# Performance work log

Measured on AMD Instinct MI355X. Metric: run time of the kernel, lower is better.

Reference implementation:

```python
import jax, jax.numpy as jnp
import numpy as np

N_NODES = 100000


def setup_inputs() -> dict:
    key = jax.random.key(0)
    k1, k2, k3, k4, k5 = jax.random.split(key, 5)
    n_edges = 1600000
    d_in, d_out = 128, 128
    input_features = jax.random.normal(k1, (N_NODES, d_in), dtype=jnp.float32)
    weight = jax.random.normal(k2, (d_in, d_out), dtype=jnp.float32) * (1.0 / np.sqrt(d_out))
    edge_vals = jax.random.uniform(k3, (n_edges,), dtype=jnp.float32)
    edge_src = jax.random.randint(k4, (n_edges,), 0, N_NODES, dtype=jnp.int32)
    edge_dst = jax.random.randint(k5, (n_edges,), 0, N_NODES, dtype=jnp.int32)
    return {
        "input_features": input_features,
        "weight": weight,
        "edge_vals": edge_vals,
        "edge_src": edge_src,
        "edge_dst": edge_dst,
    }


def reference(input_features, weight, edge_vals, edge_src, edge_dst):
    neg_slope = 0.0
    # dense transform: support = X @ W  -> [N, d_out]
    support = input_features @ weight
    # sparse SpMM: out[dst] += val * support[src]  (COO adjacency)
    msgs = edge_vals[:, None] * support[edge_src]  # [E, d_out]
    output = jax.ops.segment_sum(msgs, edge_dst, num_segments=N_NODES)
    # leaky_relu with negative_slope = neg_slope (0 -> relu)
    return jnp.where(output >= 0, output, neg_slope * output)
```

## Files before the change

### kernel.cpp

```cpp
#include <hip/hip_runtime.h>
#include <hip/hip_bf16.h>


#define D 128
#define NB_SHIFT 6
#define BNODES 64
#define MAXB 2048
#define CAPB 1408
#define RPT 6
#define XSTR 136
#define NFILL 256
#define GROWS 128

using bf16x8 = __attribute__((ext_vector_type(8))) short;
using f32x4  = __attribute__((ext_vector_type(4))) float;

__device__ inline unsigned short f2bf(float f) {
    unsigned u = __float_as_uint(f);
    u += 0x7fffu + ((u >> 16) & 1u);
    return (unsigned short)(u >> 16);
}

__global__ __launch_bounds__(256) void wtrans(const float* __restrict__ W,
                                              unsigned short* __restrict__ WT,
                                              int* cursor, int nb) {
    const int t = threadIdx.x, b = blockIdx.x;
    const int n  = (b << 4) | (t & 15);
    const int k0 = (t >> 4) << 3;
#pragma unroll
    for (int k = k0; k < k0 + 8; ++k)
        WT[n * D + k] = f2bf(W[k * D + n]);
    if (b == 0)
        for (int i = t; i < nb; i += 256) cursor[i] = 0;
}

#define SMEM_BYTES (GROWS * XSTR * 2 + 128 * XSTR * 2 + GROWS * 4)

__device__ void gemm_path(const float* __restrict__ X,
                          const unsigned short* __restrict__ WT,
                          unsigned char* __restrict__ S8,
                          float* __restrict__ scaleArr,
                          int nRows, int blk, char* smem) {
    unsigned short* Xl = (unsigned short*)smem;
    unsigned short* Wl = (unsigned short*)(smem + GROWS * XSTR * 2);
    int* rowAmaxI = (int*)(smem + GROWS * XSTR * 2 + 128 * XSTR * 2);

    const int t = threadIdx.x;
    const int row0 = blk * GROWS;

    if (t < GROWS) rowAmaxI[t] = 0;

    const uint4* WT4 = (const uint4*)WT;
    uint4* Wl4 = (uint4*)Wl;
#pragma unroll
    for (int i = t; i < 2048; i += 1024) {
        int n = i >> 4, kc8 = i & 15;
        Wl4[n * (XSTR / 8) + kc8] = WT4[i];
    }

    const float4* X4 = (const float4*)X;
    ushort4* Xl4 = (ushort4*)Xl;
#pragma unroll
    for (int i = t; i < 4096; i += 1024) {
        int r = i >> 5, c = i & 31;
        int gr = row0 + r;
        float4 v = make_float4(0.f, 0.f, 0.f, 0.f);
        if (gr < nRows) v = X4[(size_t)gr * 32 + c];
        ushort4 p;
        p.x = f2bf(v.x); p.y = f2bf(v.y); p.z = f2bf(v.z); p.w = f2bf(v.w);
        Xl4[r * (XSTR / 4) + c] = p;
    }
    __syncthreads();

    const int wv = t >> 6, lane = t & 63;
    const int m = lane & 15, quad = lane >> 4;
    const int m0  = (wv & 7) << 4;
    const int nt0 = (wv >> 3) << 2;

    f32x4 acc[4];
    f32x4 z = {0.f, 0.f, 0.f, 0.f};
#pragma unroll
    for (int nt = 0; nt < 4; ++nt) acc[nt] = z;

#pragma unroll
    for (int kc = 0; kc < 4; ++kc) {
        bf16x8 a = *(const bf16x8*)(Xl + (m0 + m) * XSTR + kc * 32 + quad * 8);
#pragma unroll
        for (int nt = 0; nt < 4; ++nt) {
            bf16x8 b = *(const bf16x8*)(Wl + ((nt0 + nt) * 16 + m) * XSTR + kc * 32 + quad * 8);
            acc[nt] = __builtin_amdgcn_mfma_f32_16x16x32_bf16(a, b, acc[nt], 0, 0, 0);
        }
    }

#pragma unroll
    for (int r = 0; r < 4; ++r) {
        float lm = fabsf(acc[0][r]);
        lm = fmaxf(lm, fabsf(acc[1][r]));
        lm = fmaxf(lm, fabsf(acc[2][r]));
        lm = fmaxf(lm, fabsf(acc[3][r]));
        atomicMax(&rowAmaxI[m0 + quad * 4 + r], __float_as_int(lm));
    }
    __syncthreads();

#pragma unroll
    for (int r = 0; r < 4; ++r) {
        const int row = m0 + quad * 4 + r;
        const int gr = row0 + row;
        const float rm = __int_as_float(rowAmaxI[row]);
        const float inv = rm > 0.f ? 127.f / rm : 0.f;
        if (gr < nRows) {
#pragma unroll
            for (int nt = 0; nt < 4; ++nt) {
                int q = __float2int_rn(acc[nt][r] * inv) + 128;
                S8[(size_t)gr * D + (nt0 + nt) * 16 + m] = (unsigned char)q;
            }
            if (m == 0 && nt0 == 0)
                scaleArr[gr] = rm * (1.f / 127.f);
        }
    }
}

__device__ void fill2_path(const int* __restrict__ src,
                           const int* __restrict__ dst,
                           const float* __restrict__ vals,
                           int* gcursor, int2* __restrict__ epk,
                           int E, int nb, int blk, char* smem) {
    int* h   = (int*)smem;
    int* cur = (int*)(smem + MAXB * 4);
    const int t = threadIdx.x;
    for (int i = t; i < nb; i += 1024) h[i] = 0;
    __syncthreads();

    int chunk = (E + NFILL - 1) / NFILL;
    chunk = (chunk + 3) & ~3;
    const int s0 = min(E, blk * chunk);
    const int s1 = min(E, s0 + chunk);
    const int vend = s0 + ((s1 - s0) & ~3);

    const int e0 = s0 + (t << 2);
    const int e1 = e0 + 4096;
    int4 rs0, rd0, rs1, rd1;
    float4 rv0, rv1;
    const bool has0 = (e0 + 4 <= vend);
    const bool has1 = (e1 + 4 <= vend);
    if (has0) {
        rd0 = *(const int4*)(dst + e0);
        rs0 = *(const int4*)(src + e0);
        rv0 = *(const float4*)(vals + e0);
        atomicAdd(&h[rd0.x >> NB_SHIFT], 1);
        atomicAdd(&h[rd0.y >> NB_SHIFT], 1);
        atomicAdd(&h[rd0.z >> NB_SHIFT], 1);
        atomicAdd(&h[rd0.w >> NB_SHIFT], 1);
    }
    if (has1) {
        rd1 = *(const int4*)(dst + e1);
        rs1 = *(const int4*)(src + e1);
        rv1 = *(const float4*)(vals + e1);
        atomicAdd(&h[rd1.x >> NB_SHIFT], 1);
        atomicAdd(&h[rd1.y >> NB_SHIFT], 1);
        atomicAdd(&h[rd1.z >> NB_SHIFT], 1);
        atomicAdd(&h[rd1.w >> NB_SHIFT], 1);
    }
    for (int e = vend + t; e < s1; e += 1024)
        atomicAdd(&h[dst[e] >> NB_SHIFT], 1);
    __syncthreads();

    for (int i = t; i < nb; i += 1024) {
        int c = h[i];
        cur[i] = c ? (i * CAPB + atomicAdd(&gcursor[i], c)) : 0;
    }
    __syncthreads();

    if (has0) {
        int p0 = atomicAdd(&cur[rd0.x >> NB_SHIFT], 1);
        int p1 = atomicAdd(&cur[rd0.y >> NB_SHIFT], 1);
        int p2 = atomicAdd(&cur[rd0.z >> NB_SHIFT], 1);
        int p3 = atomicAdd(&cur[rd0.w >> NB_SHIFT], 1);
        epk[p0] = make_int2(rs0.x | ((rd0.x & (BNODES - 1)) << 20), __float_as_int(rv0.x));
        epk[p1] = make_int2(rs0.y | ((rd0.y & (BNODES - 1)) << 20), __float_as_int(rv0.y));
        epk[p2] = make_int2(rs0.z | ((rd0.z & (BNODES - 1)) << 20), __float_as_int(rv0.z));
        epk[p3] = make_int2(rs0.w | ((rd0.w & (BNODES - 1)) << 20), __float_as_int(rv0.w));
    }
    if (has1) {
        int p0 = atomicAdd(&cur[rd1.x >> NB_SHIFT], 1);
        int p1 = atomicAdd(&cur[rd1.y >> NB_SHIFT], 1);
        int p2 = atomicAdd(&cur[rd1.z >> NB_SHIFT], 1);
        int p3 = atomicAdd(&cur[rd1.w >> NB_SHIFT], 1);
        epk[p0] = make_int2(rs1.x | ((rd1.x & (BNODES - 1)) << 20), __float_as_int(rv1.x));
        epk[p1] = make_int2(rs1.y | ((rd1.y & (BNODES - 1)) << 20), __float_as_int(rv1.y));
        epk[p2] = make_int2(rs1.z | ((rd1.z & (BNODES - 1)) << 20), __float_as_int(rv1.z));
        epk[p3] = make_int2(rs1.w | ((rd1.w & (BNODES - 1)) << 20), __float_as_int(rv1.w));
    }
    for (int e = vend + t; e < s1; e += 1024) {
        int d = dst[e];
        int pos = atomicAdd(&cur[d >> NB_SHIFT], 1);
        epk[pos] = make_int2(src[e] | ((d & (BNODES - 1)) << 20), __float_as_int(vals[e]));
    }
}

__global__ __launch_bounds__(1024, 8) void fused_pre(const float* __restrict__ X,
                                                     const unsigned short* __restrict__ WT,
                                                     unsigned char* __restrict__ S8,
                                                     float* __restrict__ scaleArr,
                                                     int nRows,
                                                     const int* __restrict__ src,
                                                     const int* __restrict__ dst,
                                                     const float* __restrict__ vals,
                                                     int* gcursor, int2* __restrict__ epk,
                                                     int E, int nb) {
    __shared__ char smem[SMEM_BYTES];
    const int bid = blockIdx.x;
    if (bid < NFILL)
        fill2_path(src, dst, vals, gcursor, epk, E, nb, bid, smem);
    else
        gemm_path(X, WT, S8, scaleArr, nRows, bid - NFILL, smem);
}

#define ACCQ(vs, mm) {                                                        \
    a[0] = fmaf(vs, (float)((mm.x) & 0xffu), a[0]);                           \
    a[1] = fmaf(vs, (float)((mm.x >> 8) & 0xffu), a[1]);                      \
    a[2] = fmaf(vs, (float)((mm.x >> 16) & 0xffu), a[2]);                     \
    a[3] = fmaf(vs, (float)(mm.x >> 24), a[3]);                               \
    a[4] = fmaf(vs, (float)((mm.y) & 0xffu), a[4]);                           \
    a[5] = fmaf(vs, (float)((mm.y >> 8) & 0xffu), a[5]);                      \
    a[6] = fmaf(vs, (float)((mm.y >> 16) & 0xffu), a[6]);                     \
    a[7] = fmaf(vs, (float)(mm.y >> 24), a[7]); }

__global__ __launch_bounds__(256, 8) void bucket_gather(const unsigned char* __restrict__ S8,
                                                        const float* __restrict__ scaleArr,
                                                        const int* __restrict__ gcursor,
                                                        const int2* __restrict__ epk,
                                                        float* __restrict__ out, int N, int nb) {
    __shared__ int2 se[CAPB];
    __shared__ int  hist[BNODES];
    __shared__ int  rows[BNODES];
    __shared__ int  cur[BNODES];

    const int t    = threadIdx.x;
    const int grp  = blockIdx.x >> 4;
    const int rem  = blockIdx.x & 15;
    const int half = rem >> 3;
    const int b    = (grp << 3) + (rem & 7);
    if (b >= nb) return;
    const int cnt  = min(gcursor[b], CAPB);
    const int beg  = b * CAPB;

    if (t < BNODES) hist[t] = 0;
    __syncthreads();

    int2 r[RPT];
#pragma unroll
    for (int i = 0; i < RPT; ++i) {
        int idx = t + (i << 8);
        if (idx < cnt) r[i] = epk[beg + idx];
    }
#pragma unroll
    for (int i = 0; i < RPT; ++i) {
        int idx = t + (i << 8);
        if (idx < cnt) atomicAdd(&hist[(r[i].x >> 20) & (BNODES - 1)], 1);
    }
    __syncthreads();

    if (t < BNODES) rows[t] = hist[t];
    __syncthreads();
#pragma unroll
    for (int off = 1; off < BNODES; off <<= 1) {
        int v = 0;
        if (t < BNODES && t >= off) v = rows[t - off];
        __syncthreads();
        if (t < BNODES && t >= off) rows[t] += v;
        __syncthreads();
    }
    if (t < BNODES) cur[t] = rows[t] - hist[t];
    __syncthreads();

#pragma unroll
    for (int i = 0; i < RPT; ++i) {
        int idx = t + (i << 8);
        if (idx < cnt) {
            int pos = atomicAdd(&cur[(r[i].x >> 20) & (BNODES - 1)], 1);
            se[pos] = r[i];
        }
    }
    __syncthreads();

    const int g = t >> 3, lane = t & 7;
    const int node0 = b << NB_SHIFT;
    const int cb = (half << 6) + (lane << 3);
    float4* o4 = (float4*)out;

#pragma unroll
    for (int nn = g; nn < BNODES; nn += 32) {
        const int send = rows[nn];
        const int sbeg = send - hist[nn];

        float a[8];
#pragma unroll
        for (int k = 0; k < 8; ++k) a[k] = 0.f;
        float svs = 0.f;

        int j = sbeg;
        for (; j + 4 <= send; j += 4) {
            int2 e0 = se[j], e1 = se[j + 1], e2 = se[j + 2], e3 = se[j + 3];
            const int s0i = e0.x & 0xFFFFF, s1i = e1.x & 0xFFFFF;
            const int s2i = e2.x & 0xFFFFF, s3i = e3.x & 0xFFFFF;
            uint2 m0 = *(const uint2*)(S8 + ((size_t)s0i << 7) + cb);
            uint2 m1 = *(const uint2*)(S8 + ((size_t)s1i << 7) + cb);
            uint2 m2 = *(const uint2*)(S8 + ((size_t)s2i << 7) + cb);
            uint2 m3 = *(const uint2*)(S8 + ((size_t)s3i << 7) + cb);
            float vs0 = __int_as_float(e0.y) * scaleArr[s0i];
            float vs1 = __int_as_float(e1.y) * scaleArr[s1i];
            float vs2 = __int_as_float(e2.y) * scaleArr[s2i];
            float vs3 = __int_as_float(e3.y) * scaleArr[s3i];
            svs += (vs0 + vs1) + (vs2 + vs3);
            ACCQ(vs0, m0); ACCQ(vs1, m1); ACCQ(vs2, m2); ACCQ(vs3, m3);
        }
        for (; j < send; ++j) {
            int2 e0 = se[j];
            const int s0i = e0.x & 0xFFFFF;
            uint2 m0 = *(const uint2*)(S8 + ((size_t)s0i << 7) + cb);
            float vs0 = __int_as_float(e0.y) * scaleArr[s0i];
            svs += vs0;
            ACCQ(vs0, m0);
        }

#pragma unroll
        for (int k = 0; k < 8; ++k) a[k] = fmaf(-128.f, svs, a[k]);

        const int gn = node0 + nn;
        if (gn < N) {
            size_t base = (size_t)gn * 32 + (half << 4) + 2 * lane;
            float4 lo = make_float4(fmaxf(a[0], 0.f), fmaxf(a[1], 0.f),
                                    fmaxf(a[2], 0.f), fmaxf(a[3], 0.f));
            float4 hi = make_float4(fmaxf(a[4], 0.f), fmaxf(a[5], 0.f),
                                    fmaxf(a[6], 0.f), fmaxf(a[7], 0.f));
            o4[base]     = lo;
            o4[base + 1] = hi;
        }
    }
}

extern "C" void kernel_launch(void* const* d_in, const int* in_sizes, int n_in,
                              void* d_out, int out_size, void* d_ws, size_t ws_size,
                              hipStream_t stream) {
    const float* X    = (const float*)d_in[0];
    const float* W    = (const float*)d_in[1];
    const float* vals = (const float*)d_in[2];
    const int*   src  = (const int*)d_in[3];
    const int*   dst  = (const int*)d_in[4];
    float*       out  = (float*)d_out;

    const int N  = in_sizes[0] / D;
    const int E  = in_sizes[2];
    const int nb = (N + BNODES - 1) / BNODES;

    size_t off = 0;
    auto take = [&](size_t bytes) {
        size_t p = off;
        off = (off + bytes + 255) & ~(size_t)255;
        return p;
    };
    char* ws = (char*)d_ws;
    size_t o_support = take((size_t)N * D);
    size_t o_scale   = take((size_t)N * sizeof(float));
    size_t o_wt      = take((size_t)D * D * sizeof(unsigned short));
    size_t o_cursor  = take((size_t)nb * sizeof(int));
    size_t o_epk     = take(((size_t)nb * CAPB + 1024) * sizeof(int2));
    (void)ws_size;

    unsigned char*  S8       = (unsigned char*)(ws + o_support);
    float*          scaleArr = (float*)(ws + o_scale);
    unsigned short* WT       = (unsigned short*)(ws + o_wt);
    int*  cursor = (int*)(ws + o_cursor);
    int2* epk    = (int2*)(ws + o_epk);

    wtrans<<<8, 256, 0, stream>>>(W, WT, cursor, nb);

    const int nbG = (N + GROWS - 1) / GROWS;
    fused_pre<<<NFILL + nbG, 1024, 0, stream>>>(X, WT, S8, scaleArr, N,
                                                src, dst, vals, cursor, epk, E, nb);

    const int gblocks = ((nb + 7) / 8) * 16;
    bucket_gather<<<gblocks, 256, 0, stream>>>(S8, scaleArr, cursor, epk, out, N, nb);
}
```

Measured before the change: 192.2 us.

## Drop LDS staging in fused GEMM path and shrink fused_pre blocks to 512 threads

The GEMM path no longer stages X and W through shared memory. Each wave now loads its 16 X rows straight from global memory, converts them to bf16 in registers, and computes all 128 output columns. B fragments are read directly from the transposed W in global or cache, and the per-row absmax is found with lane shuffles instead of LDS atomics and block barriers. Shared memory shrinks to the fill path's histogram and fused_pre moves to 512-thread blocks, with NFILL raised to 272 and each fill thread handling three int4 edge groups so the block still covers its chunk. The aim is to remove barriers and LDS traffic and raise occupancy, at the cost of repeated W reads from cache and more accumulator registers per wave.

```diff
diff --git a/kernel.cpp b/kernel.cpp
--- a/kernel.cpp
+++ b/kernel.cpp
@@ -8,8 +8,7 @@
 #define MAXB 2048
 #define CAPB 1408
 #define RPT 6
-#define XSTR 136
-#define NFILL 256
+#define NFILL 272
 #define GROWS 128
 
 using bf16x8 = __attribute__((ext_vector_type(8))) short;
@@ -34,60 +33,40 @@
         for (int i = t; i < nb; i += 256) cursor[i] = 0;
 }
 
-#define SMEM_BYTES (GROWS * XSTR * 2 + 128 * XSTR * 2 + GROWS * 4)
+#define SMEM_BYTES (MAXB * 8)
 
 __device__ void gemm_path(const float* __restrict__ X,
                           const unsigned short* __restrict__ WT,
                           unsigned char* __restrict__ S8,
                           float* __restrict__ scaleArr,
-                          int nRows, int blk, char* smem) {
-    unsigned short* Xl = (unsigned short*)smem;
-    unsigned short* Wl = (unsigned short*)(smem + GROWS * XSTR * 2);
-    int* rowAmaxI = (int*)(smem + GROWS * XSTR * 2 + 128 * XSTR * 2);
-
+                          int nRows, int blk) {
     const int t = threadIdx.x;
-    const int row0 = blk * GROWS;
-
-    if (t < GROWS) rowAmaxI[t] = 0;
-
-    const uint4* WT4 = (const uint4*)WT;
-    uint4* Wl4 = (uint4*)Wl;
-#pragma unroll
-    for (int i = t; i < 2048; i += 1024) {
-        int n = i >> 4, kc8 = i & 15;
-        Wl4[n * (XSTR / 8) + kc8] = WT4[i];
-    }
-
-    const float4* X4 = (const float4*)X;
-    ushort4* Xl4 = (ushort4*)Xl;
-#pragma unroll
-    for (int i = t; i < 4096; i += 1024) {
-        int r = i >> 5, c = i & 31;
-        int gr = row0 + r;
-        float4 v = make_float4(0.f, 0.f, 0.f, 0.f);
-        if (gr < nRows) v = X4[(size_t)gr * 32 + c];
-        ushort4 p;
-        p.x = f2bf(v.x); p.y = f2bf(v.y); p.z = f2bf(v.z); p.w = f2bf(v.w);
-        Xl4[r * (XSTR / 4) + c] = p;
-    }
-    __syncthreads();
-
     const int wv = t >> 6, lane = t & 63;
     const int m = lane & 15, quad = lane >> 4;
-    const int m0  = (wv & 7) << 4;
-    const int nt0 = (wv >> 3) << 2;
-
-    f32x4 acc[4];
+    const int row0 = blk * GROWS + (wv << 4);
+    const int ga = row0 + m;
+
+    f32x4 acc[8];
     f32x4 z = {0.f, 0.f, 0.f, 0.f};
 #pragma unroll
-    for (int nt = 0; nt < 4; ++nt) acc[nt] = z;
-
+    for (int nt = 0; nt < 8; ++nt) acc[nt] = z;
+
+    const float4* X4 = (const float4*)X;
 #pragma unroll
     for (int kc = 0; kc < 4; ++kc) {
-        bf16x8 a = *(const bf16x8*)(Xl + (m0 + m) * XSTR + kc * 32 + quad * 8);
-#pragma unroll
-        for (int nt = 0; nt < 4; ++nt) {
-            bf16x8 b = *(const bf16x8*)(Wl + ((nt0 + nt) * 16 + m) * XSTR + kc * 32 + quad * 8);
+        float4 xa = make_float4(0.f, 0.f, 0.f, 0.f), xb = xa;
+        if (ga < nRows) {
+            xa = X4[(size_t)ga * 32 + kc * 8 + quad * 2];
+            xb = X4[(size_t)ga * 32 + kc * 8 + quad * 2 + 1];
+        }
+        bf16x8 a;
+        a[0] = (short)f2bf(xa.x); a[1] = (short)f2bf(xa.y);
+        a[2] = (short)f2bf(xa.z); a[3] = (short)f2bf(xa.w);
+        a[4] = (short)f2bf(xb.x); a[5] = (short)f2bf(xb.y);
+        a[6] = (short)f2bf(xb.z); a[7] = (short)f2bf(xb.w);
+#pragma unroll
+        for (int nt = 0; nt < 8; ++nt) {
+            bf16x8 b = *(const bf16x8*)(WT + (nt * 16 + m) * D + kc * 32 + quad * 8);
             acc[nt] = __builtin_amdgcn_mfma_f32_16x16x32_bf16(a, b, acc[nt], 0, 0, 0);
         }
     }
@@ -95,27 +74,21 @@
 #pragma unroll
     for (int r = 0; r < 4; ++r) {
         float lm = fabsf(acc[0][r]);
-        lm = fmaxf(lm, fabsf(acc[1][r]));
-        lm = fmaxf(lm, fabsf(acc[2][r]));
-        lm = fmaxf(lm, fabsf(acc[3][r]));
-        atomicMax(&rowAmaxI[m0 + quad * 4 + r], __float_as_int(lm));
-    }
-    __syncthreads();
-
-#pragma unroll
-    for (int r = 0; r < 4; ++r) {
-        const int row = m0 + quad * 4 + r;
-        const int gr = row0 + row;
-        const float rm = __int_as_float(rowAmaxI[row]);
-        const float inv = rm > 0.f ? 127.f / rm : 0.f;
+#pragma unroll
+        for (int nt = 1; nt < 8; ++nt) lm = fmaxf(lm, fabsf(acc[nt][r]));
+        lm = fmaxf(lm, __shfl_xor(lm, 1));
+        lm = fmaxf(lm, __shfl_xor(lm, 2));
+        lm = fmaxf(lm, __shfl_xor(lm, 4));
+        lm = fmaxf(lm, __shfl_xor(lm, 8));
+        const int gr = row0 + (quad << 2) + r;
+        const float inv = lm > 0.f ? 127.f / lm : 0.f;
         if (gr < nRows) {
 #pragma unroll
-            for (int nt = 0; nt < 4; ++nt) {
+            for (int nt = 0; nt < 8; ++nt) {
                 int q = __float2int_rn(acc[nt][r] * inv) + 128;
-                S8[(size_t)gr * D + (nt0 + nt) * 16 + m] = (unsigned char)q;
+                S8[(size_t)gr * D + nt * 16 + m] = (unsigned char)q;
             }
-            if (m == 0 && nt0 == 0)
-                scaleArr[gr] = rm * (1.f / 127.f);
+            if (m == 0) scaleArr[gr] = lm * (1.f / 127.f);
         }
     }
 }
@@ -128,7 +101,7 @@
     int* h   = (int*)smem;
     int* cur = (int*)(smem + MAXB * 4);
     const int t = threadIdx.x;
-    for (int i = t; i < nb; i += 1024) h[i] = 0;
+    for (int i = t; i < nb; i += 512) h[i] = 0;
     __syncthreads();
 
     int chunk = (E + NFILL - 1) / NFILL;
@@ -138,11 +111,13 @@
     const int vend = s0 + ((s1 - s0) & ~3);
 
     const int e0 = s0 + (t << 2);
-    const int e1 = e0 + 4096;
-    int4 rs0, rd0, rs1, rd1;
-    float4 rv0, rv1;
+    const int e1 = e0 + 2048;
+    const int e2 = e1 + 2048;
+    int4 rs0, rd0, rs1, rd1, rs2, rd2;
+    float4 rv0, rv1, rv2;
     const bool has0 = (e0 + 4 <= vend);
     const bool has1 = (e1 + 4 <= vend);
+    const bool has2 = (e2 + 4 <= vend);
     if (has0) {
         rd0 = *(const int4*)(dst + e0);
         rs0 = *(const int4*)(src + e0);
@@ -161,11 +136,20 @@
         atomicAdd(&h[rd1.z >> NB_SHIFT], 1);
         atomicAdd(&h[rd1.w >> NB_SHIFT], 1);
     }
-    for (int e = vend + t; e < s1; e += 1024)
+    if (has2) {
+        rd2 = *(const int4*)(dst + e2);
+        rs2 = *(const int4*)(src + e2);
+        rv2 = *(const float4*)(vals + e2);
+        atomicAdd(&h[rd2.x >> NB_SHIFT], 1);
+        atomicAdd(&h[rd2.y >> NB_SHIFT], 1);
+        atomicAdd(&h[rd2.z >> NB_SHIFT], 1);
+        atomicAdd(&h[rd2.w >> NB_SHIFT], 1);
+    }
+    for (int e = vend + t; e < s1; e += 512)
         atomicAdd(&h[dst[e] >> NB_SHIFT], 1);
     __syncthreads();
 
-    for (int i = t; i < nb; i += 1024) {
+    for (int i = t; i < nb; i += 512) {
         int c = h[i];
         cur[i] = c ? (i * CAPB + atomicAdd(&gcursor[i], c)) : 0;
     }
@@ -191,29 +175,39 @@
         epk[p2] = make_int2(rs1.z | ((rd1.z & (BNODES - 1)) << 20), __float_as_int(rv1.z));
         epk[p3] = make_int2(rs1.w | ((rd1.w & (BNODES - 1)) << 20), __float_as_int(rv1.w));
     }
-    for (int e = vend + t; e < s1; e += 1024) {
+    if (has2) {
+        int p0 = atomicAdd(&cur[rd2.x >> NB_SHIFT], 1);
+        int p1 = atomicAdd(&cur[rd2.y >> NB_SHIFT], 1);
+        int p2 = atomicAdd(&cur[rd2.z >> NB_SHIFT], 1);
+        int p3 = atomicAdd(&cur[rd2.w >> NB_SHIFT], 1);
+        epk[p0] = make_int2(rs2.x | ((rd2.x & (BNODES - 1)) << 20), __float_as_int(rv2.x));
+        epk[p1] = make_int2(rs2.y | ((rd2.y & (BNODES - 1)) << 20), __float_as_int(rv2.y));
+        epk[p2] = make_int2(rs2.z | ((rd2.z & (BNODES - 1)) << 20), __float_as_int(rv2.z));
+        epk[p3] = make_int2(rs2.w | ((rd2.w & (BNODES - 1)) << 20), __float_as_int(rv2.w));
+    }
+    for (int e = vend + t; e < s1; e += 512) {
         int d = dst[e];
         int pos = atomicAdd(&cur[d >> NB_SHIFT], 1);
         epk[pos] = make_int2(src[e] | ((d & (BNODES - 1)) << 20), __float_as_int(vals[e]));
     }
 }
 
-__global__ __launch_bounds__(1024, 8) void fused_pre(const float* __restrict__ X,
-                                                     const unsigned short* __restrict__ WT,
-                                                     unsigned char* __restrict__ S8,
-                                                     float* __restrict__ scaleArr,
-                                                     int nRows,
-                                                     const int* __restrict__ src,
-                                                     const int* __restrict__ dst,
-                                                     const float* __restrict__ vals,
-                                                     int* gcursor, int2* __restrict__ epk,
-                                                     int E, int nb) {
+__global__ __launch_bounds__(512, 6) void fused_pre(const float* __restrict__ X,
+                                                    const unsigned short* __restrict__ WT,
+                                                    unsigned char* __restrict__ S8,
+                                                    float* __restrict__ scaleArr,
+                                                    int nRows,
+                                                    const int* __restrict__ src,
+                                                    const int* __restrict__ dst,
+                                                    const float* __restrict__ vals,
+                                                    int* gcursor, int2* __restrict__ epk,
+                                                    int E, int nb) {
     __shared__ char smem[SMEM_BYTES];
     const int bid = blockIdx.x;
     if (bid < NFILL)
         fill2_path(src, dst, vals, gcursor, epk, E, nb, bid, smem);
     else
-        gemm_path(X, WT, S8, scaleArr, nRows, bid - NFILL, smem);
+        gemm_path(X, WT, S8, scaleArr, nRows, bid - NFILL);
 }
 
 #define ACCQ(vs, mm) {                                                        \
@@ -377,8 +371,8 @@
     wtrans<<<8, 256, 0, stream>>>(W, WT, cursor, nb);
 
     const int nbG = (N + GROWS - 1) / GROWS;
-    fused_pre<<<NFILL + nbG, 1024, 0, stream>>>(X, WT, S8, scaleArr, N,
-                                                src, dst, vals, cursor, epk, E, nb);
+    fused_pre<<<NFILL + nbG, 512, 0, stream>>>(X, WT, S8, scaleArr, N,
+                                               src, dst, vals, cursor, epk, E, nb);
 
     const int gblocks = ((nb + 7) / 8) * 16;
     bucket_gather<<<gblocks, 256, 0, stream>>>(S8, scaleArr, cursor, epk, out, N, nb);
```

After: 205.5 us. 6.9% more time.
